# Kernel optimization log

Hardware: AMD Instinct MI355X
Metric: run time of the kernel (lower is better)

Reference implementation:

```python
import jax, jax.numpy as jnp
import numpy as np

B = 1024
M = 131072          # memory_size
K = 256             # key_dim
CHOOSE_K = 256
BETA = 1e-08
EPS = 0.001


def setup_inputs() -> dict:
    key = jax.random.key(0)
    k1, k2, k3 = jax.random.split(key, 3)
    q = jax.random.normal(k1, (B, K), dtype=jnp.float32)
    mk = jax.random.normal(k2, (M, K), dtype=jnp.float32)
    memory_key = mk / jnp.linalg.norm(mk, axis=1, keepdims=True)  # unit-norm keys as in update_memory
    # __init__: first half values = 1 (real), second half = 0 (fake)
    memory_values = jnp.concatenate([jnp.ones((M // 2,), jnp.float32),
                                     jnp.zeros((M - M // 2,), jnp.float32)])
    # hist starts near 1e-5; add small positive noise so p_c is non-degenerate
    memory_hist = 1e-05 + 1e-05 * jax.random.uniform(k3, (M,), dtype=jnp.float32)
    return {"q": q, "memory_key": memory_key,
            "memory_values": memory_values, "memory_hist": memory_hist}


def reference(q, memory_key, memory_values, memory_hist):
    # similarities: [B, M]
    similarities = jnp.matmul(q, memory_key.T)
    p_x_given_c_unnorm = jnp.exp(similarities)
    hist_b = memory_hist + BETA
    p_c = hist_b / jnp.sum(hist_b)                       # [M]
    p_c_given_x = p_x_given_c_unnorm * p_c               # [B, M]
    p_c_given_x_approx, idxs = jax.lax.top_k(p_c_given_x, CHOOSE_K)  # [B, k]
    vals = memory_values[idxs]                           # gather, [B, k]
    p_y_given_x_unnorm = jnp.sum(vals * p_c_given_x_approx, axis=1)
    p_y_given_x = p_y_given_x_unnorm / jnp.sum(p_c_given_x_approx, axis=1)
    return jnp.clip(p_y_given_x, EPS, 1.0 - EPS)
```

## Files before the change

### kernel.cpp

```cpp
#include <hip/hip_runtime.h>
#include <math.h>
#include <stdint.h>

#define MMEM 131072
#define KDIM 256
#define NB   1024
#define TOPK 256
#define BETA_F 1e-08f
#define NTILE 2048
#define OVFCAP 65536
#define SLOTS 4
#define SBINS 1024
#define SCAP  2560
#define SBCAP 256

typedef _Float16 f16x8 __attribute__((ext_vector_type(8)));
typedef float    f32x4 __attribute__((ext_vector_type(4)));

__device__ __forceinline__ void gload16(const void* g, void* l) {
  __builtin_amdgcn_global_load_lds(
      (const __attribute__((address_space(1))) uint32_t*)g,
      (__attribute__((address_space(3))) uint32_t*)l, 16, 0, 0);
}

#define NQ16 (NB * KDIM / 16)
#define NM16 (MMEM * KDIM / 16)
#define CVTB ((NQ16 + NM16) / 256)
__global__ __launch_bounds__(256) void prep_kernel(const float* __restrict__ q,
                                                   const float* __restrict__ mk,
                                                   _Float16* __restrict__ qh,
                                                   _Float16* __restrict__ mkh,
                                                   const float* __restrict__ hist,
                                                   float* __restrict__ partials,
                                                   float* __restrict__ partials_log) {
  const int b = blockIdx.x;
  if (b < CVTB) {
    int i = b * 256 + threadIdx.x;
    const float* in; _Float16* out; size_t j;
    if (i < NQ16) { in = q;  out = qh;  j = (size_t)i; }
    else          { in = mk; out = mkh; j = (size_t)(i - NQ16); }
    const float4* src = (const float4*)(in + j * 16);
    union { _Float16 h[16]; uint4 u[2]; } p;
    #pragma unroll
    for (int k = 0; k < 4; ++k) {
      float4 v = src[k];
      p.h[k * 4 + 0] = (_Float16)v.x; p.h[k * 4 + 1] = (_Float16)v.y;
      p.h[k * 4 + 2] = (_Float16)v.z; p.h[k * 4 + 3] = (_Float16)v.w;
    }
    uint4* dst = (uint4*)(out + j * 16);
    dst[0] = p.u[0];
    dst[1] = p.u[1];
    return;
  }
  const int bid = b - CVTB;
  float s = 0.f, sl = 0.f;
  for (int i = bid * 256 + threadIdx.x; i < MMEM; i += 256 * 256) {
    float h = hist[i] + BETA_F;
    s += h;
    sl += logf(h);
  }
  #pragma unroll
  for (int off = 32; off > 0; off >>= 1) {
    s  += __shfl_down(s, off);
    sl += __shfl_down(sl, off);
  }
  __shared__ float ws[4], wsl[4];
  int lane = threadIdx.x & 63, wid = threadIdx.x >> 6;
  if (lane == 0) { ws[wid] = s; wsl[wid] = sl; }
  __syncthreads();
  if (threadIdx.x == 0) {
    partials[bid]     = ws[0] + ws[1] + ws[2] + ws[3];
    partials_log[bid] = wsl[0] + wsl[1] + wsl[2] + wsl[3];
  }
}

__global__ __launch_bounds__(256) void logpc_final_kernel(const float* __restrict__ hist,
                                                          const float* __restrict__ partials,
                                                          const float* __restrict__ partials_log,
                                                          float* __restrict__ logpc,
                                                          float* __restrict__ out_sum,
                                                          float* __restrict__ out_thresh,
                                                          uint32_t* __restrict__ ovf_cnt,
                                                          float z0) {
  __shared__ float ws[4], wsl[4];
  const int tid = threadIdx.x;
  float s = partials[tid];
  float sl = (blockIdx.x == 0) ? partials_log[tid] : 0.f;
  #pragma unroll
  for (int off = 32; off > 0; off >>= 1) {
    s  += __shfl_down(s, off);
    sl += __shfl_down(sl, off);
  }
  int lane = tid & 63, wid = tid >> 6;
  if (lane == 0) { ws[wid] = s; wsl[wid] = sl; }
  __syncthreads();
  const float sum = ws[0] + ws[1] + ws[2] + ws[3];
  const int i = blockIdx.x * 256 + tid;
  logpc[i] = logf(hist[i] + BETA_F) - logf(sum);
  if (blockIdx.x == 0 && tid == 0) {
    float suml = wsl[0] + wsl[1] + wsl[2] + wsl[3];
    *out_sum = sum;
    *out_thresh = suml / (float)MMEM - logf(sum) + z0;
    *ovf_cnt = 0u;
  }
}

__global__ __launch_bounds__(256, 3) void gemm_kernel(const _Float16* __restrict__ qh,
                                                      const _Float16* __restrict__ mkh,
                                                      const float* __restrict__ logpc,
                                                      const float* __restrict__ values,
                                                      const float* __restrict__ thresh,
                                                      float2* __restrict__ cand,
                                                      uint8_t* __restrict__ cnt,
                                                      int4* __restrict__ ovf,
                                                      uint32_t* __restrict__ ovf_cnt,
                                                      int wgoff) {
  __shared__ _Float16 As[3][4096];
  __shared__ _Float16 Bs[3][4096];

  const int t    = threadIdx.x;
  const int lane = t & 63;
  const int wave = t >> 6;
  const int wr   = (wave & 1) * 64;
  const int wc   = (wave >> 1) * 64;
  const int lm   = lane & 15;
  const int lk   = lane >> 4;

  const int wg  = blockIdx.x + wgoff;
  const int lg  = ((wg & 7) << 10) | (wg >> 3);
  const int row0 = (lg & 7) << 7;
  const int col0 = (lg >> 3) << 7;

  const int r0q = t >> 2;
  const int cc  = (t & 3) ^ ((r0q >> 1) & 3);

  const char* gA0 = (const char*)qh  + ((size_t)(row0 + r0q)      * KDIM) * 2 + cc * 16;
  const char* gA1 = (const char*)qh  + ((size_t)(row0 + 64 + r0q) * KDIM) * 2 + cc * 16;
  const char* gB0 = (const char*)mkh + ((size_t)(col0 + r0q)      * KDIM) * 2 + cc * 16;
  const char* gB1 = (const char*)mkh + ((size_t)(col0 + 64 + r0q) * KDIM) * 2 + cc * 16;

  int offA[4], offB[4];
  #pragma unroll
  for (int i = 0; i < 4; ++i) {
    int ar = wr + i * 16 + lm;
    offA[i] = ar * 64 + ((lk ^ ((ar >> 1) & 3)) * 16);
    int br = wc + i * 16 + lm;
    offB[i] = br * 64 + ((lk ^ ((br >> 1) & 3)) * 16);
  }

  const float tv = *thresh;
  float lpv[4], vv[4];
  #pragma unroll
  for (int j = 0; j < 4; ++j) {
    lpv[j] = logpc[col0 + wc + j * 16 + lm];
    vv[j]  = values[col0 + wc + j * 16 + lm];
  }
  asm volatile("s_waitcnt vmcnt(0)" ::: "memory");

  f32x4 acc[4][4];
  #pragma unroll
  for (int i = 0; i < 4; i++)
    #pragma unroll
    for (int j = 0; j < 4; j++)
      acc[i][j] = (f32x4){0.f, 0.f, 0.f, 0.f};

  auto stage = [&](int buf, int chunk) {
    const size_t ko = (size_t)chunk * 64;
    gload16(gA0 + ko, (char*)&As[buf][0] + t * 16);
    gload16(gA1 + ko, (char*)&As[buf][0] + 4096 + t * 16);
    gload16(gB0 + ko, (char*)&Bs[buf][0] + t * 16);
    gload16(gB1 + ko, (char*)&Bs[buf][0] + 4096 + t * 16);
  };

  stage(0, 0);
  stage(1, 1);
  asm volatile("s_waitcnt vmcnt(4)" ::: "memory");
  __builtin_amdgcn_s_barrier();
  asm volatile("" ::: "memory");

  #pragma unroll
  for (int it = 0; it < 8; ++it) {
    const int cur = it % 3;
    const char* Ab = (const char*)&As[cur][0];
    const char* Bb = (const char*)&Bs[cur][0];
    f16x8 af[4], bf[4];
    #pragma unroll
    for (int i = 0; i < 4; ++i) af[i] = *(const f16x8*)(Ab + offA[i]);
    #pragma unroll
    for (int j = 0; j < 4; ++j) bf[j] = *(const f16x8*)(Bb + offB[j]);
    if (it + 2 < 8) stage((it + 2) % 3, it + 2);
    __builtin_amdgcn_s_setprio(1);
    #pragma unroll
    for (int i = 0; i < 4; ++i)
      #pragma unroll
      for (int j = 0; j < 4; ++j)
        acc[i][j] = __builtin_amdgcn_mfma_f32_16x16x32_f16(af[i], bf[j], acc[i][j], 0, 0, 0);
    __builtin_amdgcn_s_setprio(0);
    if (it < 7) {
      if (it + 2 < 8) asm volatile("s_waitcnt vmcnt(4)" ::: "memory");
      else            asm volatile("s_waitcnt vmcnt(0)" ::: "memory");
      __builtin_amdgcn_s_barrier();
      asm volatile("" ::: "memory");
    }
  }

  const int coltile = (col0 + wc) >> 6;
  const uint32_t ltm = (1u << lm) - 1u;
  const int shift = lane & 48;
  #pragma unroll
  for (int i = 0; i < 4; ++i) {
    #pragma unroll
    for (int r4 = 0; r4 < 4; ++r4) {
      const int row = row0 + wr + i * 16 + lk * 4 + r4;
      float sv[4];
      uint32_t gm[4];
      int tot = 0;
      #pragma unroll
      for (int j = 0; j < 4; ++j) {
        sv[j] = acc[i][j][r4] + lpv[j];
        gm[j] = (uint32_t)((__ballot(sv[j] >= tv) >> shift) & 0xFFFFull);
        tot += __popc(gm[j]);
      }
      const size_t bucket = (size_t)row * NTILE + coltile;
      if (lm == 0) cnt[bucket] = (uint8_t)(tot < SLOTS ? tot : SLOTS);
      if (tot) {
        float2* bs = cand + bucket * SLOTS;
        int prev = 0;
        #pragma unroll
        for (int j = 0; j < 4; ++j) {
          if ((gm[j] >> lm) & 1u) {
            int k = prev + __popc(gm[j] & ltm);
            if (k < SLOTS) {
              bs[k] = make_float2(sv[j], vv[j]);
            } else {
              int col = col0 + wc + j * 16 + lm;
              uint32_t p = atomicAdd(ovf_cnt, 1u);
              if (p < OVFCAP) ovf[p] = make_int4(row, col, __float_as_int(sv[j]),
                                                 __float_as_int(vv[j]));
            }
          }
          prev += __popc(gm[j]);
        }
      }
    }
  }
}

__global__ __launch_bounds__(512) void select_kernel(const float2* __restrict__ cand,
                                                     const uint8_t* __restrict__ cnt,
                                                     const int4* __restrict__ ovf,
                                                     const uint32_t* __restrict__ ovf_cnt,
                                                     const float* __restrict__ thresh,
                                                     float* __restrict__ out) {
  __shared__ uint32_t hist[SBINS];
  __shared__ float cs_s[SCAP];
  __shared__ float cs_v[SCAP];
  __shared__ uint32_t csum[32];
  __shared__ int s_bstar, s_above, s_ccnt, s_bcnt;
  __shared__ float bin_s[SBCAP];
  __shared__ float bin_v[SBCAP];
  __shared__ float red_p[8], red_vp[8];

  const int tid = threadIdx.x;
  const int row = blockIdx.x;
  const float tv = *thresh;
  const int novf = (int)min(*ovf_cnt, (uint32_t)OVFCAP);

  for (int i = tid; i < SBINS; i += 512) hist[i] = 0;
  if (tid == 0) { s_ccnt = 0; s_bcnt = 0; }
  __syncthreads();

  {
    const uint32_t* cnt32 = (const uint32_t*)(cnt + (size_t)row * NTILE);
    for (int w = tid; w < NTILE / 4; w += 512) {
      uint32_t cw = cnt32[w];
      if (cw == 0u) continue;
      #pragma unroll
      for (int s4 = 0; s4 < 4; ++s4) {
        int c = (int)((cw >> (8 * s4)) & 0xFFu);
        if (c > 0) {
          size_t bucket = (size_t)row * NTILE + (w * 4 + s4);
          const float4* b4 = (const float4*)(cand + bucket * SLOTS);
          float4 lo = b4[0];
          float4 hi = b4[1];
          #pragma unroll
          for (int k = 0; k < 4; k++) {
            if (k < c) {
              float s = (k == 0) ? lo.x : (k == 1) ? lo.z : (k == 2) ? hi.x : hi.z;
              float v = (k == 0) ? lo.y : (k == 1) ? lo.w : (k == 2) ? hi.y : hi.w;
              int b = (int)((s - tv) * 256.0f);
              b = b < 0 ? 0 : (b > SBINS - 1 ? SBINS - 1 : b);
              atomicAdd(&hist[b], 1u);
              int pos = atomicAdd(&s_ccnt, 1);
              if (pos < SCAP) { cs_s[pos] = s; cs_v[pos] = v; }
            }
          }
        }
      }
    }
  }
  for (int i = tid; i < novf; i += 512) {
    int4 e = ovf[i];
    if (e.x == row) {
      float s = __int_as_float(e.z);
      float v = __int_as_float(e.w);
      int b = (int)((s - tv) * 256.0f);
      b = b < 0 ? 0 : (b > SBINS - 1 ? SBINS - 1 : b);
      atomicAdd(&hist[b], 1u);
      int pos = atomicAdd(&s_ccnt, 1);
      if (pos < SCAP) { cs_s[pos] = s; cs_v[pos] = v; }
    }
  }
  __syncthreads();

  if (tid < 32) {
    uint32_t s = 0;
    for (int b = 0; b < 32; b++) s += hist[tid * 32 + b];
    csum[tid] = s;
  }
  __syncthreads();
  if (tid == 0) {
    uint32_t cum = 0;
    int bstar = 0; uint32_t above = 0;
    for (int c = 31; c >= 0; c--) {
      if (cum + csum[c] >= TOPK) {
        for (int b = 31; b >= 0; b--) {
          uint32_t h = hist[c * 32 + b];
          if (cum + h >= TOPK) { bstar = c * 32 + b; above = cum; goto found; }
          cum += h;
        }
      }
      cum += csum[c];
    }
    bstar = 0; above = cum - hist[0];
  found:
    s_bstar = bstar;
    s_above = (int)above;
  }
  __syncthreads();
  const int bstar = s_bstar;
  int rneed = TOPK - s_above;
  const int ctot = s_ccnt;

  float psum = 0.f, vpsum = 0.f;
  if (ctot <= SCAP) {
    for (int i = tid; i < ctot; i += 512) {
      float s = cs_s[i];
      float v = cs_v[i];
      int b = (int)((s - tv) * 256.0f);
      b = b < 0 ? 0 : (b > SBINS - 1 ? SBINS - 1 : b);
      if (b > bstar) {
        float p = __expf(s);
        psum += p;
        vpsum += p * v;
      } else if (b == bstar) {
        int pos = atomicAdd(&s_bcnt, 1);
        if (pos < SBCAP) { bin_s[pos] = s; bin_v[pos] = v; }
      }
    }
  } else {
    for (int tile = tid; tile < NTILE; tile += 512) {
      size_t bucket = (size_t)row * NTILE + tile;
      int c = (int)cnt[bucket];
      const float2* bs = cand + bucket * SLOTS;
      for (int k = 0; k < c; k++) {
        float2 e = bs[k];
        int b = (int)((e.x - tv) * 256.0f);
        b = b < 0 ? 0 : (b > SBINS - 1 ? SBINS - 1 : b);
        if (b > bstar) {
          float p = __expf(e.x);
          psum += p;
          vpsum += p * e.y;
        } else if (b == bstar) {
          int pos = atomicAdd(&s_bcnt, 1);
          if (pos < SBCAP) { bin_s[pos] = e.x; bin_v[pos] = e.y; }
        }
      }
    }
    for (int i = tid; i < novf; i += 512) {
      int4 e = ovf[i];
      if (e.x == row) {
        float s = __int_as_float(e.z);
        float v = __int_as_float(e.w);
        int b = (int)((s - tv) * 256.0f);
        b = b < 0 ? 0 : (b > SBINS - 1 ? SBINS - 1 : b);
        if (b > bstar) {
          float p = __expf(s);
          psum += p;
          vpsum += p * v;
        } else if (b == bstar) {
          int pos = atomicAdd(&s_bcnt, 1);
          if (pos < SBCAP) { bin_s[pos] = s; bin_v[pos] = v; }
        }
      }
    }
  }
  __syncthreads();

  int c2 = s_bcnt < SBCAP ? s_bcnt : SBCAP;
  int n2 = 1;
  while (n2 < c2) n2 <<= 1;
  for (int i = c2 + tid; i < n2; i += 512) { bin_s[i] = -INFINITY; bin_v[i] = 0.f; }
  __syncthreads();

  for (int size = 2; size <= n2; size <<= 1) {
    for (int stride = size >> 1; stride > 0; stride >>= 1) {
      for (int i = tid; i < n2; i += 512) {
        int j = i ^ stride;
        if (j > i) {
          float si = bin_s[i], sj = bin_s[j];
          float vi = bin_v[i], vj = bin_v[j];
          bool igt = (si > sj) || (si == sj && vi > vj);
          bool desc = ((i & size) == 0);
          if (desc ? !igt : igt) {
            bin_s[i] = sj; bin_s[j] = si;
            bin_v[i] = vj; bin_v[j] = vi;
          }
        }
      }
      __syncthreads();
    }
  }

  int take = rneed < c2 ? rneed : c2;
  if (take < 0) take = 0;
  for (int i = tid; i < take; i += 512) {
    float p = __expf(bin_s[i]);
    psum += p;
    vpsum += p * bin_v[i];
  }

  #pragma unroll
  for (int off = 32; off > 0; off >>= 1) {
    psum  += __shfl_down(psum, off);
    vpsum += __shfl_down(vpsum, off);
  }
  int lane = tid & 63, wid = tid >> 6;
  if (lane == 0) { red_p[wid] = psum; red_vp[wid] = vpsum; }
  __syncthreads();
  if (tid == 0) {
    float P = 0.f, V = 0.f;
    for (int w = 0; w < 8; w++) { P += red_p[w]; V += red_vp[w]; }
    float r = V / P;
    r = fminf(fmaxf(r, 1e-3f), 1.0f - 1e-3f);
    out[row] = r;
  }
}

extern "C" void kernel_launch(void* const* d_in, const int* in_sizes, int n_in,
                              void* d_out, int out_size, void* d_ws, size_t ws_size,
                              hipStream_t stream) {
  const float* q      = (const float*)d_in[0];
  const float* mk     = (const float*)d_in[1];
  const float* values = (const float*)d_in[2];
  const float* hist   = (const float*)d_in[3];
  float* out = (float*)d_out;

  float*    ws_sum   = (float*)d_ws;
  float*    ws_thr   = (float*)((char*)d_ws + 64);
  uint32_t* ovf_cnt  = (uint32_t*)((char*)d_ws + 128);
  float*    partials = (float*)((char*)d_ws + 4096);
  float*    partialsl= (float*)((char*)d_ws + 8192);
  float*    logpc    = (float*)((char*)d_ws + 16384);
  _Float16* qh       = (_Float16*)((char*)d_ws + 540672);
  _Float16* mkh      = (_Float16*)((char*)d_ws + 1064960);
  uint8_t*  cnt      = (uint8_t*)((char*)d_ws + 68173824ull);
  int4*     ovf      = (int4*)((char*)d_ws + 76562432ull);
  float2*   cand     = (float2*)((char*)d_ws + 77611008ull);

  const float z0 = 2.4176f;

  prep_kernel<<<CVTB + 256, 256, 0, stream>>>(q, mk, qh, mkh, hist, partials, partialsl);
  logpc_final_kernel<<<MMEM / 256, 256, 0, stream>>>(hist, partials, partialsl, logpc,
                                                     ws_sum, ws_thr, ovf_cnt, z0);
  gemm_kernel<<<4096, 256, 0, stream>>>(qh, mkh, logpc, values, ws_thr,
                                        cand, cnt, ovf, ovf_cnt, 0);
  gemm_kernel<<<4096, 256, 0, stream>>>(qh, mkh, logpc, values, ws_thr,
                                        cand, cnt, ovf, ovf_cnt, 4096);
  select_kernel<<<NB, 512, 0, stream>>>(cand, cnt, ovf, ovf_cnt, ws_thr, out);
}
```

Baseline: 359.3 us.

## Make GEMM persistent with 16 column tiles per block and cross-tile prefetch

Replaces two launches of 4096 one-tile blocks with a single launch of 512 blocks, each looping over 16 column tiles for a fixed row block. The A tile stays L2-hot, and the triple-buffered pipeline prefetches the next tile's first chunks during the current tile's tail, so there is no per-tile prologue bubble. logpc and values for all 16 tiles are staged into LDS up front. Occupancy bound drops to 2 waves per SIMD, and 512 blocks on 256 CUs may give less latency hiding and some load imbalance.

Result: slower. 368.2 us (+2.5%).

```diff
diff --git a/kernel.cpp b/kernel.cpp
--- a/kernel.cpp
+++ b/kernel.cpp
@@ -105,7 +105,7 @@
   }
 }
 
-__global__ __launch_bounds__(256, 3) void gemm_kernel(const _Float16* __restrict__ qh,
+__global__ __launch_bounds__(256, 2) void gemm_kernel(const _Float16* __restrict__ qh,
                                                       const _Float16* __restrict__ mkh,
                                                       const float* __restrict__ logpc,
                                                       const float* __restrict__ values,
@@ -113,10 +113,11 @@
                                                       float2* __restrict__ cand,
                                                       uint8_t* __restrict__ cnt,
                                                       int4* __restrict__ ovf,
-                                                      uint32_t* __restrict__ ovf_cnt,
-                                                      int wgoff) {
+                                                      uint32_t* __restrict__ ovf_cnt) {
   __shared__ _Float16 As[3][4096];
   __shared__ _Float16 Bs[3][4096];
+  __shared__ float lpvL[16 * 128];
+  __shared__ float vvL[16 * 128];
 
   const int t    = threadIdx.x;
   const int lane = t & 63;
@@ -126,18 +127,19 @@
   const int lm   = lane & 15;
   const int lk   = lane >> 4;
 
-  const int wg  = blockIdx.x + wgoff;
-  const int lg  = ((wg & 7) << 10) | (wg >> 3);
-  const int row0 = (lg & 7) << 7;
-  const int col0 = (lg >> 3) << 7;
+  const int b    = blockIdx.x;
+  const int xcd  = b & 7;
+  const int l    = b >> 3;
+  const int row0 = (l & 7) << 7;
+  const int ct0  = xcd * 128 + (l >> 3);
 
   const int r0q = t >> 2;
   const int cc  = (t & 3) ^ ((r0q >> 1) & 3);
 
-  const char* gA0 = (const char*)qh  + ((size_t)(row0 + r0q)      * KDIM) * 2 + cc * 16;
-  const char* gA1 = (const char*)qh  + ((size_t)(row0 + 64 + r0q) * KDIM) * 2 + cc * 16;
-  const char* gB0 = (const char*)mkh + ((size_t)(col0 + r0q)      * KDIM) * 2 + cc * 16;
-  const char* gB1 = (const char*)mkh + ((size_t)(col0 + 64 + r0q) * KDIM) * 2 + cc * 16;
+  const char* gA0 = (const char*)qh + ((size_t)(row0 + r0q) * KDIM) * 2 + cc * 16;
+  const char* gA1 = gA0 + (size_t)64 * KDIM * 2;
+  const char* gB0 = (const char*)mkh + ((size_t)(ct0 * 128 + r0q) * KDIM) * 2 + cc * 16;
+  const char* gB1 = gB0 + (size_t)64 * KDIM * 2;
 
   int offA[4], offB[4];
   #pragma unroll
@@ -149,97 +151,122 @@
   }
 
   const float tv = *thresh;
-  float lpv[4], vv[4];
+  asm volatile("s_waitcnt vmcnt(0)" ::: "memory");
+
+  auto stage = [&](int buf, int sidx, int cidx) {
+    const size_t aofs = (size_t)cidx * 64;
+    const size_t bofs = (size_t)sidx * 524288 + aofs;
+    char* Ad = (char*)As + buf * 8192 + t * 16;
+    char* Bd = (char*)Bs + buf * 8192 + t * 16;
+    gload16(gA0 + aofs, Ad);
+    gload16(gA1 + aofs, Ad + 4096);
+    gload16(gB0 + bofs, Bd);
+    gload16(gB1 + bofs, Bd + 4096);
+  };
+
   #pragma unroll
-  for (int j = 0; j < 4; ++j) {
-    lpv[j] = logpc[col0 + wc + j * 16 + lm];
-    vv[j]  = values[col0 + wc + j * 16 + lm];
-  }
-  asm volatile("s_waitcnt vmcnt(0)" ::: "memory");
-
-  f32x4 acc[4][4];
-  #pragma unroll
-  for (int i = 0; i < 4; i++)
-    #pragma unroll
-    for (int j = 0; j < 4; j++)
-      acc[i][j] = (f32x4){0.f, 0.f, 0.f, 0.f};
-
-  auto stage = [&](int buf, int chunk) {
-    const size_t ko = (size_t)chunk * 64;
-    gload16(gA0 + ko, (char*)&As[buf][0] + t * 16);
-    gload16(gA1 + ko, (char*)&As[buf][0] + 4096 + t * 16);
-    gload16(gB0 + ko, (char*)&Bs[buf][0] + t * 16);
-    gload16(gB1 + ko, (char*)&Bs[buf][0] + 4096 + t * 16);
-  };
-
-  stage(0, 0);
-  stage(1, 1);
+  for (int r = 0; r < 2; ++r) {
+    int s = r * 8 + (t >> 5);
+    size_t col0s = (size_t)(ct0 + s * 8) * 128;
+    int o = (t & 31) * 16;
+    gload16((const char*)(logpc + col0s) + o, (char*)lpvL + s * 512 + o);
+    gload16((const char*)(values + col0s) + o, (char*)vvL + s * 512 + o);
+  }
+  stage(0, 0, 0);
+  stage(1, 0, 1);
   asm volatile("s_waitcnt vmcnt(4)" ::: "memory");
   __builtin_amdgcn_s_barrier();
   asm volatile("" ::: "memory");
 
-  #pragma unroll
-  for (int it = 0; it < 8; ++it) {
-    const int cur = it % 3;
-    const char* Ab = (const char*)&As[cur][0];
-    const char* Bb = (const char*)&Bs[cur][0];
-    f16x8 af[4], bf[4];
-    #pragma unroll
-    for (int i = 0; i < 4; ++i) af[i] = *(const f16x8*)(Ab + offA[i]);
-    #pragma unroll
-    for (int j = 0; j < 4; ++j) bf[j] = *(const f16x8*)(Bb + offB[j]);
-    if (it + 2 < 8) stage((it + 2) % 3, it + 2);
-    __builtin_amdgcn_s_setprio(1);
-    #pragma unroll
-    for (int i = 0; i < 4; ++i)
-      #pragma unroll
-      for (int j = 0; j < 4; ++j)
-        acc[i][j] = __builtin_amdgcn_mfma_f32_16x16x32_f16(af[i], bf[j], acc[i][j], 0, 0, 0);
-    __builtin_amdgcn_s_setprio(0);
-    if (it < 7) {
-      if (it + 2 < 8) asm volatile("s_waitcnt vmcnt(4)" ::: "memory");
-      else            asm volatile("s_waitcnt vmcnt(0)" ::: "memory");
-      __builtin_amdgcn_s_barrier();
-      asm volatile("" ::: "memory");
-    }
-  }
-
-  const int coltile = (col0 + wc) >> 6;
   const uint32_t ltm = (1u << lm) - 1u;
   const int shift = lane & 48;
-  #pragma unroll
-  for (int i = 0; i < 4; ++i) {
+  int cur = 0;
+
+  for (int s = 0; s < 16; ++s) {
+    f32x4 acc[4][4];
     #pragma unroll
-    for (int r4 = 0; r4 < 4; ++r4) {
-      const int row = row0 + wr + i * 16 + lk * 4 + r4;
-      float sv[4];
-      uint32_t gm[4];
-      int tot = 0;
+    for (int i = 0; i < 4; i++)
       #pragma unroll
-      for (int j = 0; j < 4; ++j) {
-        sv[j] = acc[i][j][r4] + lpv[j];
-        gm[j] = (uint32_t)((__ballot(sv[j] >= tv) >> shift) & 0xFFFFull);
-        tot += __popc(gm[j]);
-      }
-      const size_t bucket = (size_t)row * NTILE + coltile;
-      if (lm == 0) cnt[bucket] = (uint8_t)(tot < SLOTS ? tot : SLOTS);
-      if (tot) {
-        float2* bs = cand + bucket * SLOTS;
-        int prev = 0;
+      for (int j = 0; j < 4; j++)
+        acc[i][j] = (f32x4){0.f, 0.f, 0.f, 0.f};
+
+    #pragma unroll
+    for (int c = 0; c < 8; ++c) {
+      const char* Ab = (const char*)As + cur * 8192;
+      const char* Bb = (const char*)Bs + cur * 8192;
+      f16x8 af[4], bf[4];
+      #pragma unroll
+      for (int i = 0; i < 4; ++i) af[i] = *(const f16x8*)(Ab + offA[i]);
+      #pragma unroll
+      for (int j = 0; j < 4; ++j) bf[j] = *(const f16x8*)(Bb + offB[j]);
+      if (c < 6) {
+        int sbuf = cur + 2; if (sbuf >= 3) sbuf -= 3;
+        stage(sbuf, s, c + 2);
+      } else if (s < 15) {
+        int sbuf = cur + 2; if (sbuf >= 3) sbuf -= 3;
+        stage(sbuf, s + 1, c - 6);
+      }
+      __builtin_amdgcn_s_setprio(1);
+      #pragma unroll
+      for (int i = 0; i < 4; ++i)
+        #pragma unroll
+        for (int j = 0; j < 4; ++j)
+          acc[i][j] = __builtin_amdgcn_mfma_f32_16x16x32_f16(af[i], bf[j], acc[i][j], 0, 0, 0);
+      __builtin_amdgcn_s_setprio(0);
+      if (s < 15 || c < 6) {
+        asm volatile("s_waitcnt vmcnt(4)" ::: "memory");
+        __builtin_amdgcn_s_barrier();
+        asm volatile("" ::: "memory");
+      } else if (c == 6) {
+        asm volatile("s_waitcnt vmcnt(0)" ::: "memory");
+        __builtin_amdgcn_s_barrier();
+        asm volatile("" ::: "memory");
+      }
+      cur = cur + 1; if (cur >= 3) cur -= 3;
+    }
+
+    const int col0s = (ct0 + s * 8) * 128;
+    const int coltile = (col0s + wc) >> 6;
+    float lpv[4], vv[4];
+    #pragma unroll
+    for (int j = 0; j < 4; ++j) {
+      lpv[j] = lpvL[s * 128 + wc + j * 16 + lm];
+      vv[j]  = vvL[s * 128 + wc + j * 16 + lm];
+    }
+    #pragma unroll
+    for (int i = 0; i < 4; ++i) {
+      #pragma unroll
+      for (int r4 = 0; r4 < 4; ++r4) {
+        const int row = row0 + wr + i * 16 + lk * 4 + r4;
+        float sv[4];
+        uint32_t gm[4];
+        int tot = 0;
         #pragma unroll
         for (int j = 0; j < 4; ++j) {
-          if ((gm[j] >> lm) & 1u) {
-            int k = prev + __popc(gm[j] & ltm);
-            if (k < SLOTS) {
-              bs[k] = make_float2(sv[j], vv[j]);
-            } else {
-              int col = col0 + wc + j * 16 + lm;
-              uint32_t p = atomicAdd(ovf_cnt, 1u);
-              if (p < OVFCAP) ovf[p] = make_int4(row, col, __float_as_int(sv[j]),
-                                                 __float_as_int(vv[j]));
+          sv[j] = acc[i][j][r4] + lpv[j];
+          gm[j] = (uint32_t)((__ballot(sv[j] >= tv) >> shift) & 0xFFFFull);
+          tot += __popc(gm[j]);
+        }
+        const size_t bucket = (size_t)row * NTILE + coltile;
+        if (lm == 0) cnt[bucket] = (uint8_t)(tot < SLOTS ? tot : SLOTS);
+        if (tot) {
+          float2* bs = cand + bucket * SLOTS;
+          int prev = 0;
+          #pragma unroll
+          for (int j = 0; j < 4; ++j) {
+            if ((gm[j] >> lm) & 1u) {
+              int k = prev + __popc(gm[j] & ltm);
+              if (k < SLOTS) {
+                bs[k] = make_float2(sv[j], vv[j]);
+              } else {
+                int col = col0s + wc + j * 16 + lm;
+                uint32_t p = atomicAdd(ovf_cnt, 1u);
+                if (p < OVFCAP) ovf[p] = make_int4(row, col, __float_as_int(sv[j]),
+                                                   __float_as_int(vv[j]));
+              }
             }
+            prev += __popc(gm[j]);
           }
-          prev += __popc(gm[j]);
         }
       }
     }
@@ -473,9 +500,7 @@
   prep_kernel<<<CVTB + 256, 256, 0, stream>>>(q, mk, qh, mkh, hist, partials, partialsl);
   logpc_final_kernel<<<MMEM / 256, 256, 0, stream>>>(hist, partials, partialsl, logpc,
                                                      ws_sum, ws_thr, ovf_cnt, z0);
-  gemm_kernel<<<4096, 256, 0, stream>>>(qh, mkh, logpc, values, ws_thr,
-                                        cand, cnt, ovf, ovf_cnt, 0);
-  gemm_kernel<<<4096, 256, 0, stream>>>(qh, mkh, logpc, values, ws_thr,
-                                        cand, cnt, ovf, ovf_cnt, 4096);
+  gemm_kernel<<<512, 256, 0, stream>>>(qh, mkh, logpc, values, ws_thr,
+                                       cand, cnt, ovf, ovf_cnt);
   select_kernel<<<NB, 512, 0, stream>>>(cand, cnt, ovf, ovf_cnt, ws_thr, out);
 }
```
